# Optimization experiments

Hardware: AMD Instinct MI355X
Metric: run time of the kernel (lower is better)

The kernel has to match this reference:

```python
import jax, jax.numpy as jnp
import numpy as np

T, D_IN, D_OUT, E, K = 4096, 1024, 1024, 8, 2
H = max(D_IN, D_OUT) * 4  # 4096, per nbHidden = max(nbIn, nbOut) * 4


def setup_inputs() -> dict:
    key = jax.random.key(0)
    ks = jax.random.split(key, 12)
    s = 0.02
    return {
        "x": jax.random.normal(ks[0], (T, D_IN), dtype=jnp.float32),
        "noise": jax.random.normal(ks[1], (T, E), dtype=jnp.float32),
        "gate_w": jax.random.normal(ks[2], (D_IN, E), dtype=jnp.float32) * s,
        "gate_b": jnp.zeros((E,), dtype=jnp.float32),
        "noise_w": jax.random.normal(ks[3], (D_IN, E), dtype=jnp.float32) * s,
        "noise_b": jnp.zeros((E,), dtype=jnp.float32),
        "w1": jax.random.normal(ks[4], (E, D_IN, H), dtype=jnp.float32) * s,
        "b1": jnp.zeros((E, H), dtype=jnp.float32),
        "w2": jax.random.normal(ks[5], (E, H, D_OUT), dtype=jnp.float32) * s,
        "b2": jnp.zeros((E, D_OUT), dtype=jnp.float32),
    }


def reference(x, noise, gate_w, gate_b, noise_w, noise_b, w1, b1, w2, b2):
    # Noisy gating: gate(x) + randn * softplus(noise(x))
    logits = (x @ gate_w + gate_b) + noise * jax.nn.softplus(x @ noise_w + noise_b)  # [T, E]
    topk_vals, topk_idx = jax.lax.top_k(logits, K)          # [T, K]
    gate_prob = jax.nn.softmax(topk_vals, axis=1)           # softmax over selected K logits
    rows = jnp.arange(x.shape[0])[:, None]
    weights = jnp.zeros((x.shape[0], E), dtype=x.dtype).at[rows, topk_idx].set(gate_prob)  # [T, E]

    # Dense path (memMode=False): run every expert MLP on all tokens, masked combine.
    h = jax.nn.relu(jnp.einsum("ti,eih->teh", x, w1) + b1[None])   # [T, E, H]
    expert_out = jnp.einsum("teh,eho->teo", h, w2) + b2[None]       # [T, E, O]
    x_out = jnp.einsum("te,teo->to", weights, expert_out)           # [T, O]
    return x_out, weights
```

## Files before the change

kernel.cpp:

```cpp
#include <hip/hip_runtime.h>

#define T_TOK 4096
#define DIN   1024
#define DOUT  1024
#define NEXP  8
#define HDIM  4096
#define RCAP  9216
#define MT128 80

typedef float f32x4 __attribute__((ext_vector_type(4)));
typedef short bf16x8 __attribute__((ext_vector_type(8)));
typedef unsigned short u16x4 __attribute__((ext_vector_type(4)));
typedef unsigned short u16x8 __attribute__((ext_vector_type(8)));

__device__ __forceinline__ float bf2f(unsigned short u) {
    union { unsigned int i; float f; } v; v.i = ((unsigned int)u) << 16; return v.f;
}
__device__ __forceinline__ unsigned short f2bf(float f) {
    union { unsigned int i; float f; } v; v.f = f;
    unsigned int r = v.i + 0x7FFFu + ((v.i >> 16) & 1u);
    return (unsigned short)(r >> 16);
}

__global__ __launch_bounds__(64) void gating_kernel(
    const float* __restrict__ x, const float* __restrict__ noise,
    const float* __restrict__ gw, const float* __restrict__ gb,
    const float* __restrict__ nw, const float* __restrict__ nb,
    float* __restrict__ wout,
    int* __restrict__ tok_e, float* __restrict__ tok_p)
{
    int t = blockIdx.x;
    int lane = threadIdx.x;
    const float* xr = x + (size_t)t * DIN;
    double ag[NEXP], an[NEXP];
#pragma unroll
    for (int e = 0; e < NEXP; ++e) { ag[e] = 0.0; an[e] = 0.0; }
    for (int d = lane; d < DIN; d += 64) {
        double xv = (double)xr[d];
        const f32x4* g4 = (const f32x4*)(gw + (size_t)d * NEXP);
        const f32x4* n4 = (const f32x4*)(nw + (size_t)d * NEXP);
        f32x4 ga = g4[0], gbv = g4[1], na = n4[0], nbv = n4[1];
#pragma unroll
        for (int j = 0; j < 4; ++j) {
            ag[j]     += xv * (double)ga[j];
            ag[4 + j] += xv * (double)gbv[j];
            an[j]     += xv * (double)na[j];
            an[4 + j] += xv * (double)nbv[j];
        }
    }
#pragma unroll
    for (int e = 0; e < NEXP; ++e) {
        double g = ag[e], n = an[e];
#pragma unroll
        for (int m = 32; m > 0; m >>= 1) { g += __shfl_xor(g, m); n += __shfl_xor(n, m); }
        ag[e] = g; an[e] = n;
    }
    double lg[NEXP];
#pragma unroll
    for (int e = 0; e < NEXP; ++e) {
        double z = an[e] + (double)nb[e];
        double sp = fmax(z, 0.0) + log1p(exp(-fabs(z)));
        lg[e] = ag[e] + (double)gb[e] + (double)noise[(size_t)t * NEXP + e] * sp;
    }
    int i0 = 0; double v0 = lg[0];
#pragma unroll
    for (int e = 1; e < NEXP; ++e) if (lg[e] > v0) { v0 = lg[e]; i0 = e; }
    int i1 = -1; double v1 = -1.0e300;
#pragma unroll
    for (int e = 0; e < NEXP; ++e) if (e != i0 && lg[e] > v1) { v1 = lg[e]; i1 = e; }
    double d1 = exp(v1 - v0);
    float p0 = (float)(1.0 / (1.0 + d1));
    float p1 = (float)(d1 / (1.0 + d1));
    if (lane < NEXP) {
        float wv = (lane == i0) ? p0 : ((lane == i1) ? p1 : 0.0f);
        wout[(size_t)t * NEXP + lane] = wv;
    }
    if (lane == 0) {
        tok_e[2 * t] = i0;     tok_e[2 * t + 1] = i1;
        tok_p[2 * t] = p0;     tok_p[2 * t + 1] = p1;
    }
}

__global__ __launch_bounds__(256) void scan_kernel(
    const int* __restrict__ tok_e, int* __restrict__ tok_slot, int* __restrict__ cnt)
{
    __shared__ int wsum[4];
    int e = blockIdx.x;
    int tid = threadIdx.x;
    int wv = tid >> 6;
    int lane = tid & 63;
    int base = 0;
    for (int c = 0; c < 2 * T_TOK; c += 256) {
        int i = c + tid;
        int m = (tok_e[i] == e) ? 1 : 0;
        unsigned long long bal = __ballot(m);
        int before = __popcll(bal & ((1ull << lane) - 1ull));
        if (lane == 0) wsum[wv] = __popcll(bal);
        __syncthreads();
        int woff = 0;
#pragma unroll
        for (int w = 0; w < 4; ++w) if (w < wv) woff += wsum[w];
        if (m) tok_slot[i] = base + woff + before;
        int tot = wsum[0] + wsum[1] + wsum[2] + wsum[3];
        __syncthreads();
        base += tot;
    }
    if (tid == 0) cnt[e] = base;
}

__global__ void prefix_kernel(const int* __restrict__ cnt, int* __restrict__ poff,
                              int* __restrict__ t2e, int* __restrict__ trow)
{
    if (threadIdx.x != 0 || blockIdx.x != 0) return;
    int base = 0, a = 0;
    for (int e = 0; e < NEXP; ++e) {
        poff[e] = base;
        int c = cnt[e];
        int nt = (c + 127) >> 7;
        for (int i = 0; i < nt; ++i) { t2e[a] = e; trow[a] = base + (i << 7); ++a; }
        base += nt << 7;
    }
    for (; a < MT128; ++a) { t2e[a] = -1; trow[a] = 0; }
}

__global__ __launch_bounds__(256) void gather_kernel(
    const float* __restrict__ x, const int* __restrict__ tok_e,
    const int* __restrict__ tok_slot, const int* __restrict__ poff,
    unsigned short* __restrict__ Xg)
{
    int b = blockIdx.x;
    int t = b >> 1, k = b & 1;
    int e = tok_e[2 * t + k];
    int row = poff[e] + tok_slot[2 * t + k];
    int c = threadIdx.x << 2;
    f32x4 v = *(const f32x4*)(x + (size_t)t * DIN + c);
    u16x4 o;
#pragma unroll
    for (int j = 0; j < 4; ++j) o[j] = f2bf(v[j]);
    *(u16x4*)(Xg + (size_t)row * DIN + c) = o;
}

__global__ __launch_bounds__(256) void convw2x_kernel(
    const float* __restrict__ w1, unsigned short* __restrict__ W1t,
    const float* __restrict__ w2, unsigned short* __restrict__ W2t)
{
    __shared__ float tile[64][65];
    int e = blockIdx.x;
    int idx = blockIdx.y;
    const float* W; unsigned short* Wt; int K, N, k0, n0;
    if (idx < 1024) {
        W = w1; Wt = W1t; K = DIN; N = HDIM;
        k0 = (idx >> 6) << 6; n0 = (idx & 63) << 6;
    } else {
        int i2 = idx - 1024;
        W = w2; Wt = W2t; K = HDIM; N = DOUT;
        k0 = (i2 >> 4) << 6; n0 = (i2 & 15) << 6;
    }
    int tid = threadIdx.x;
    const float* src = W + ((size_t)e * K + k0) * N + n0;
    int r = tid >> 4, c4 = (tid & 15) << 2;
#pragma unroll
    for (int i = 0; i < 4; ++i) {
        f32x4 v = *(const f32x4*)(src + (size_t)(r + (i << 4)) * N + c4);
        *(f32x4*)(&tile[r + (i << 4)][c4]) = v;
    }
    __syncthreads();
    unsigned short* dst = Wt + ((size_t)e * N + n0) * K + k0;
#pragma unroll
    for (int i = 0; i < 2; ++i) {
        int u = (i << 8) + tid;
        int n = u >> 3, kk = (u & 7) << 3;
        u16x8 o;
#pragma unroll
        for (int q = 0; q < 8; ++q) o[q] = f2bf(tile[kk + q][n]);
        *(u16x8*)(dst + (size_t)n * K + kk) = o;
    }
}

__global__ __launch_bounds__(512, 4) void gemm1_wide_kernel(
    const unsigned short* __restrict__ A,
    const unsigned short* __restrict__ Bt,
    unsigned short* __restrict__ C,
    const float* __restrict__ bias,
    const int* __restrict__ t2e, const int* __restrict__ trow)
{
    const int lda = DIN, ldb = DIN, N = HDIM;
    int cpx = gridDim.x >> 3;
    int wg = ((blockIdx.x & 7) * cpx) + (blockIdx.x >> 3);
    int tileid = wg >> 4;
    int nb = wg & 15;
    int e = t2e[tileid];
    if (e < 0) return;
    int row0 = trow[tileid];
    int n0 = nb << 8;

    __shared__ __align__(16) unsigned short As[128 * 64];
    __shared__ __align__(16) unsigned short Bs[256 * 64];

    int tid = threadIdx.x;
    int lane = tid & 63;
    int wv = tid >> 6;
    int wr = (wv >> 2) << 6;
    int wc = (wv & 3) << 6;

    const unsigned short* Ab = A + (size_t)row0 * lda;
    const unsigned short* Bb = Bt + ((size_t)e * N + n0) * ldb;

    f32x4 acc[4][4] = {};
    int hr = lane & 15;
    int q4 = lane >> 4;

    for (int kt = 0; kt < 16; ++kt) {
        __syncthreads();
        int kb = kt << 6;
#pragma unroll
        for (int i = 0; i < 2; ++i) {
            int u = (i << 9) + tid;
            int r = u >> 3, sp = u & 7;
            int col = ((sp ^ (r & 7)) << 3);
            __builtin_amdgcn_global_load_lds(
                (const __attribute__((address_space(1))) void*)(Ab + (size_t)r * lda + kb + col),
                (__attribute__((address_space(3))) void*)(&As[u << 3]), 16, 0, 0);
        }
#pragma unroll
        for (int i = 0; i < 4; ++i) {
            int u = (i << 9) + tid;
            int r = u >> 3, sp = u & 7;
            int col = ((sp ^ (r & 7)) << 3);
            __builtin_amdgcn_global_load_lds(
                (const __attribute__((address_space(1))) void*)(Bb + (size_t)r * ldb + kb + col),
                (__attribute__((address_space(3))) void*)(&Bs[u << 3]), 16, 0, 0);
        }
        __syncthreads();
#pragma unroll
        for (int kq = 0; kq < 2; ++kq) {
            int slog = (kq << 2) | q4;
            bf16x8 af[4], bfv[4];
#pragma unroll
            for (int m = 0; m < 4; ++m) {
                int r = wr + (m << 4) + hr;
                af[m] = *(const bf16x8*)(&As[(r << 6) + ((slog ^ (r & 7)) << 3)]);
            }
#pragma unroll
            for (int n = 0; n < 4; ++n) {
                int r = wc + (n << 4) + hr;
                bfv[n] = *(const bf16x8*)(&Bs[(r << 6) + ((slog ^ (r & 7)) << 3)]);
            }
#pragma unroll
            for (int m = 0; m < 4; ++m)
#pragma unroll
                for (int n = 0; n < 4; ++n)
                    acc[m][n] = __builtin_amdgcn_mfma_f32_16x16x32_bf16(af[m], bfv[n], acc[m][n], 0, 0, 0);
        }
    }

    int rq = q4 << 2;
    int cl = hr;
#pragma unroll
    for (int n = 0; n < 4; ++n) {
        int col = wc + (n << 4) + cl;
        float bv = bias[(size_t)e * N + n0 + col];
#pragma unroll
        for (int m = 0; m < 4; ++m) {
#pragma unroll
            for (int r = 0; r < 4; ++r) {
                int row = wr + (m << 4) + rq + r;
                float v = acc[m][n][r] + bv;
                v = fmaxf(v, 0.0f);
                C[(size_t)(row0 + row) * N + n0 + col] = f2bf(v);
            }
        }
    }
}

__global__ __launch_bounds__(256, 4) void gemm64_kernel(
    const unsigned short* __restrict__ A, int lda,
    const unsigned short* __restrict__ Bt, int ldb, int N, int KLEN,
    unsigned short* __restrict__ C,
    const float* __restrict__ bias,
    const int* __restrict__ t2e, const int* __restrict__ trow,
    int nbshift, int relu)
{
    int nwg = gridDim.x;
    int cpx = nwg >> 3;
    int wg = ((blockIdx.x & 7) * cpx) + (blockIdx.x >> 3);
    int tileid = wg >> nbshift;
    int nb = wg & ((1 << nbshift) - 1);

    int e = t2e[tileid];
    if (e < 0) return;
    int row0 = trow[tileid];
    int n0 = nb << 7;

    __shared__ __align__(16) unsigned short As[128 * 64];
    __shared__ __align__(16) unsigned short Bs[128 * 64];

    int tid = threadIdx.x;
    int lane = tid & 63;
    int wv = tid >> 6;
    int wr = (wv >> 1) << 6;
    int wc = (wv & 1) << 6;

    const unsigned short* Ab = A + (size_t)row0 * lda;
    const unsigned short* Bb = Bt + ((size_t)e * N + n0) * ldb;

    f32x4 acc[4][4] = {};

    int sr_lo = tid >> 3;
    int sp = tid & 7;
    int hr = lane & 15;
    int q4 = lane >> 4;

    int nkt = KLEN >> 6;
    for (int kt = 0; kt < nkt; ++kt) {
        __syncthreads();
        int kb = kt << 6;
#pragma unroll
        for (int i = 0; i < 4; ++i) {
            int r = (i << 5) + sr_lo;
            int col = ((sp ^ (r & 7)) << 3);
            int u = (i << 8) + tid;
            __builtin_amdgcn_global_load_lds(
                (const __attribute__((address_space(1))) void*)(Ab + (size_t)r * lda + kb + col),
                (__attribute__((address_space(3))) void*)(&As[u << 3]), 16, 0, 0);
            __builtin_amdgcn_global_load_lds(
                (const __attribute__((address_space(1))) void*)(Bb + (size_t)r * ldb + kb + col),
                (__attribute__((address_space(3))) void*)(&Bs[u << 3]), 16, 0, 0);
        }
        __syncthreads();
#pragma unroll
        for (int kq = 0; kq < 2; ++kq) {
            int slog = (kq << 2) | q4;
            bf16x8 af[4], bfv[4];
#pragma unroll
            for (int m = 0; m < 4; ++m) {
                int r = wr + (m << 4) + hr;
                af[m] = *(const bf16x8*)(&As[(r << 6) + ((slog ^ (r & 7)) << 3)]);
            }
#pragma unroll
            for (int n = 0; n < 4; ++n) {
                int r = wc + (n << 4) + hr;
                bfv[n] = *(const bf16x8*)(&Bs[(r << 6) + ((slog ^ (r & 7)) << 3)]);
            }
#pragma unroll
            for (int m = 0; m < 4; ++m)
#pragma unroll
                for (int n = 0; n < 4; ++n)
                    acc[m][n] = __builtin_amdgcn_mfma_f32_16x16x32_bf16(af[m], bfv[n], acc[m][n], 0, 0, 0);
        }
    }

    int rq = q4 << 2;
    int cl = hr;
#pragma unroll
    for (int n = 0; n < 4; ++n) {
        int col = wc + (n << 4) + cl;
        float bv = bias[(size_t)e * N + n0 + col];
#pragma unroll
        for (int m = 0; m < 4; ++m) {
#pragma unroll
            for (int r = 0; r < 4; ++r) {
                int row = wr + (m << 4) + rq + r;
                float v = acc[m][n][r] + bv;
                if (relu) v = fmaxf(v, 0.0f);
                C[(size_t)(row0 + row) * N + n0 + col] = f2bf(v);
            }
        }
    }
}

__global__ __launch_bounds__(256) void combine_kernel(
    const unsigned short* __restrict__ O, const int* __restrict__ tok_e,
    const int* __restrict__ tok_slot, const float* __restrict__ tok_p,
    const int* __restrict__ poff, float* __restrict__ xout)
{
    int t = blockIdx.x;
    int e0 = tok_e[2 * t], e1 = tok_e[2 * t + 1];
    int r0 = poff[e0] + tok_slot[2 * t];
    int r1 = poff[e1] + tok_slot[2 * t + 1];
    float p0 = tok_p[2 * t], p1 = tok_p[2 * t + 1];
    int c = threadIdx.x << 2;
    u16x4 a = *(const u16x4*)(O + (size_t)r0 * DOUT + c);
    u16x4 b = *(const u16x4*)(O + (size_t)r1 * DOUT + c);
    f32x4 r;
#pragma unroll
    for (int j = 0; j < 4; ++j) r[j] = p0 * bf2f(a[j]) + p1 * bf2f(b[j]);
    *(f32x4*)(xout + (size_t)t * DOUT + c) = r;
}

extern "C" void kernel_launch(void* const* d_in, const int* in_sizes, int n_in,
                              void* d_out, int out_size, void* d_ws, size_t ws_size,
                              hipStream_t stream)
{
    const float* x     = (const float*)d_in[0];
    const float* noise = (const float*)d_in[1];
    const float* gw    = (const float*)d_in[2];
    const float* gb    = (const float*)d_in[3];
    const float* nw    = (const float*)d_in[4];
    const float* nb    = (const float*)d_in[5];
    const float* w1    = (const float*)d_in[6];
    const float* b1    = (const float*)d_in[7];
    const float* w2    = (const float*)d_in[8];
    const float* b2    = (const float*)d_in[9];
    float* xout = (float*)d_out;
    float* wout = xout + (size_t)T_TOK * DOUT;

    char* ws = (char*)d_ws;
    int*   cnt      = (int*)(ws + 0);
    int*   poff     = (int*)(ws + 256);
    int*   t2e      = (int*)(ws + 512);
    int*   trow     = (int*)(ws + 1024);
    int*   tok_e    = (int*)(ws + 2048);
    int*   tok_slot = (int*)(ws + 34816);
    float* tok_p    = (float*)(ws + 67584);
    size_t oXg = 104448;
    unsigned short* Xg  = (unsigned short*)(ws + oXg);
    unsigned short* O   = Xg;
    size_t oH  = oXg + (size_t)RCAP * DIN * 2;
    unsigned short* H   = (unsigned short*)(ws + oH);
    size_t oW1 = oH + (size_t)RCAP * HDIM * 2;
    unsigned short* W1t = (unsigned short*)(ws + oW1);
    size_t oW2 = oW1 + (size_t)NEXP * HDIM * DIN * 2;
    unsigned short* W2t = (unsigned short*)(ws + oW2);

    gating_kernel<<<T_TOK, 64, 0, stream>>>(x, noise, gw, gb, nw, nb,
                                            wout, tok_e, tok_p);
    scan_kernel<<<NEXP, 256, 0, stream>>>(tok_e, tok_slot, cnt);
    prefix_kernel<<<1, 1, 0, stream>>>(cnt, poff, t2e, trow);
    gather_kernel<<<2 * T_TOK, 256, 0, stream>>>(x, tok_e, tok_slot, poff, Xg);
    convw2x_kernel<<<dim3(NEXP, 2048), 256, 0, stream>>>(w1, W1t, w2, W2t);
    gemm1_wide_kernel<<<MT128 * 16, 512, 0, stream>>>(
        Xg, W1t, H, b1, t2e, trow);
    gemm64_kernel<<<MT128 * 8, 256, 0, stream>>>(
        H, HDIM, W2t, HDIM, DOUT, HDIM, O, b2, t2e, trow, 3, 0);
    combine_kernel<<<T_TOK, 256, 0, stream>>>(O, tok_e, tok_slot, tok_p, poff, xout);
}
```

Measured before the change: 335.1 us.

## Split-K the second expert GEMM and fold gating into weight-conversion kernel

The second grouped GEMM is split into two K halves, doubling its workgroup count. Each half writes bf16 partials into scratch buffers that reuse the W1t region, and the combine kernel adds them. Separately, the gating computation is folded into the weight transpose/convert kernel as extra grid rows, removing one launch and letting gating overlap with conversion. The cost is extra partial-output traffic and a second bf16 rounding of each partial sum.

```diff
diff --git a/kernel.cpp b/kernel.cpp
--- a/kernel.cpp
+++ b/kernel.cpp
@@ -22,15 +22,13 @@
     return (unsigned short)(r >> 16);
 }
 
-__global__ __launch_bounds__(64) void gating_kernel(
+__device__ __forceinline__ void gating_body(
+    int t, int lane,
     const float* __restrict__ x, const float* __restrict__ noise,
     const float* __restrict__ gw, const float* __restrict__ gb,
     const float* __restrict__ nw, const float* __restrict__ nb,
-    float* __restrict__ wout,
-    int* __restrict__ tok_e, float* __restrict__ tok_p)
-{
-    int t = blockIdx.x;
-    int lane = threadIdx.x;
+    float* __restrict__ wout, int* __restrict__ tok_e, float* __restrict__ tok_p)
+{
     const float* xr = x + (size_t)t * DIN;
     double ag[NEXP], an[NEXP];
 #pragma unroll
@@ -78,6 +76,52 @@
     if (lane == 0) {
         tok_e[2 * t] = i0;     tok_e[2 * t + 1] = i1;
         tok_p[2 * t] = p0;     tok_p[2 * t + 1] = p1;
+    }
+}
+
+__global__ __launch_bounds__(256) void prep_kernel(
+    const float* __restrict__ w1, unsigned short* __restrict__ W1t,
+    const float* __restrict__ w2, unsigned short* __restrict__ W2t,
+    const float* __restrict__ x, const float* __restrict__ noise,
+    const float* __restrict__ gw, const float* __restrict__ gb,
+    const float* __restrict__ nw, const float* __restrict__ nb,
+    float* __restrict__ wout, int* __restrict__ tok_e, float* __restrict__ tok_p)
+{
+    __shared__ float tile[64][65];
+    int yy = blockIdx.y;
+    int tid = threadIdx.x;
+    if (yy >= 2048) {
+        int t = (((yy - 2048) << 3) + blockIdx.x) * 4 + (tid >> 6);
+        gating_body(t, tid & 63, x, noise, gw, gb, nw, nb, wout, tok_e, tok_p);
+        return;
+    }
+    int e = blockIdx.x;
+    const float* W; unsigned short* Wt; int K, N, k0, n0;
+    if (yy < 1024) {
+        W = w1; Wt = W1t; K = DIN; N = HDIM;
+        k0 = (yy >> 6) << 6; n0 = (yy & 63) << 6;
+    } else {
+        int i2 = yy - 1024;
+        W = w2; Wt = W2t; K = HDIM; N = DOUT;
+        k0 = (i2 >> 4) << 6; n0 = (i2 & 15) << 6;
+    }
+    const float* src = W + ((size_t)e * K + k0) * N + n0;
+    int r = tid >> 4, c4 = (tid & 15) << 2;
+#pragma unroll
+    for (int i = 0; i < 4; ++i) {
+        f32x4 v = *(const f32x4*)(src + (size_t)(r + (i << 4)) * N + c4);
+        *(f32x4*)(&tile[r + (i << 4)][c4]) = v;
+    }
+    __syncthreads();
+    unsigned short* dst = Wt + ((size_t)e * N + n0) * K + k0;
+#pragma unroll
+    for (int i = 0; i < 2; ++i) {
+        int u = (i << 8) + tid;
+        int n = u >> 3, kk = (u & 7) << 3;
+        u16x8 o;
+#pragma unroll
+        for (int q = 0; q < 8; ++q) o[q] = f2bf(tile[kk + q][n]);
+        *(u16x8*)(dst + (size_t)n * K + kk) = o;
     }
 }
 
@@ -140,43 +184,6 @@
     *(u16x4*)(Xg + (size_t)row * DIN + c) = o;
 }
 
-__global__ __launch_bounds__(256) void convw2x_kernel(
-    const float* __restrict__ w1, unsigned short* __restrict__ W1t,
-    const float* __restrict__ w2, unsigned short* __restrict__ W2t)
-{
-    __shared__ float tile[64][65];
-    int e = blockIdx.x;
-    int idx = blockIdx.y;
-    const float* W; unsigned short* Wt; int K, N, k0, n0;
-    if (idx < 1024) {
-        W = w1; Wt = W1t; K = DIN; N = HDIM;
-        k0 = (idx >> 6) << 6; n0 = (idx & 63) << 6;
-    } else {
-        int i2 = idx - 1024;
-        W = w2; Wt = W2t; K = HDIM; N = DOUT;
-        k0 = (i2 >> 4) << 6; n0 = (i2 & 15) << 6;
-    }
-    int tid = threadIdx.x;
-    const float* src = W + ((size_t)e * K + k0) * N + n0;
-    int r = tid >> 4, c4 = (tid & 15) << 2;
-#pragma unroll
-    for (int i = 0; i < 4; ++i) {
-        f32x4 v = *(const f32x4*)(src + (size_t)(r + (i << 4)) * N + c4);
-        *(f32x4*)(&tile[r + (i << 4)][c4]) = v;
-    }
-    __syncthreads();
-    unsigned short* dst = Wt + ((size_t)e * N + n0) * K + k0;
-#pragma unroll
-    for (int i = 0; i < 2; ++i) {
-        int u = (i << 8) + tid;
-        int n = u >> 3, kk = (u & 7) << 3;
-        u16x8 o;
-#pragma unroll
-        for (int q = 0; q < 8; ++q) o[q] = f2bf(tile[kk + q][n]);
-        *(u16x8*)(dst + (size_t)n * K + kk) = o;
-    }
-}
-
 __global__ __launch_bounds__(512, 4) void gemm1_wide_kernel(
     const unsigned short* __restrict__ A,
     const unsigned short* __restrict__ Bt,
@@ -273,24 +280,27 @@
     }
 }
 
-__global__ __launch_bounds__(256, 4) void gemm64_kernel(
-    const unsigned short* __restrict__ A, int lda,
-    const unsigned short* __restrict__ Bt, int ldb, int N, int KLEN,
-    unsigned short* __restrict__ C,
+__global__ __launch_bounds__(256, 4) void gemm2_sk_kernel(
+    const unsigned short* __restrict__ A,
+    const unsigned short* __restrict__ Bt,
+    unsigned short* __restrict__ C0, unsigned short* __restrict__ C1,
     const float* __restrict__ bias,
-    const int* __restrict__ t2e, const int* __restrict__ trow,
-    int nbshift, int relu)
-{
-    int nwg = gridDim.x;
-    int cpx = nwg >> 3;
+    const int* __restrict__ t2e, const int* __restrict__ trow)
+{
+    const int lda = HDIM, ldb = HDIM, N = DOUT, KLEN = HDIM / 2;
+    int cpx = gridDim.x >> 3;
     int wg = ((blockIdx.x & 7) * cpx) + (blockIdx.x >> 3);
-    int tileid = wg >> nbshift;
-    int nb = wg & ((1 << nbshift) - 1);
+    int tileid = wg >> 4;
+    int low = wg & 15;
+    int nb = low >> 1;
+    int ks = low & 1;
 
     int e = t2e[tileid];
     if (e < 0) return;
     int row0 = trow[tileid];
     int n0 = nb << 7;
+    int koff = ks * KLEN;
+    unsigned short* C = ks ? C1 : C0;
 
     __shared__ __align__(16) unsigned short As[128 * 64];
     __shared__ __align__(16) unsigned short Bs[128 * 64];
@@ -301,8 +311,8 @@
     int wr = (wv >> 1) << 6;
     int wc = (wv & 1) << 6;
 
-    const unsigned short* Ab = A + (size_t)row0 * lda;
-    const unsigned short* Bb = Bt + ((size_t)e * N + n0) * ldb;
+    const unsigned short* Ab = A + (size_t)row0 * lda + koff;
+    const unsigned short* Bb = Bt + ((size_t)e * N + n0) * ldb + koff;
 
     f32x4 acc[4][4] = {};
 
@@ -311,8 +321,7 @@
     int hr = lane & 15;
     int q4 = lane >> 4;
 
-    int nkt = KLEN >> 6;
-    for (int kt = 0; kt < nkt; ++kt) {
+    for (int kt = 0; kt < KLEN / 64; ++kt) {
         __syncthreads();
         int kb = kt << 6;
 #pragma unroll
@@ -355,24 +364,23 @@
 #pragma unroll
     for (int n = 0; n < 4; ++n) {
         int col = wc + (n << 4) + cl;
-        float bv = bias[(size_t)e * N + n0 + col];
+        float bv = (ks == 0) ? bias[(size_t)e * N + n0 + col] : 0.0f;
 #pragma unroll
         for (int m = 0; m < 4; ++m) {
 #pragma unroll
             for (int r = 0; r < 4; ++r) {
                 int row = wr + (m << 4) + rq + r;
-                float v = acc[m][n][r] + bv;
-                if (relu) v = fmaxf(v, 0.0f);
-                C[(size_t)(row0 + row) * N + n0 + col] = f2bf(v);
+                C[(size_t)(row0 + row) * N + n0 + col] = f2bf(acc[m][n][r] + bv);
             }
         }
     }
 }
 
 __global__ __launch_bounds__(256) void combine_kernel(
-    const unsigned short* __restrict__ O, const int* __restrict__ tok_e,
-    const int* __restrict__ tok_slot, const float* __restrict__ tok_p,
-    const int* __restrict__ poff, float* __restrict__ xout)
+    const unsigned short* __restrict__ Oa, const unsigned short* __restrict__ Ob,
+    const int* __restrict__ tok_e, const int* __restrict__ tok_slot,
+    const float* __restrict__ tok_p, const int* __restrict__ poff,
+    float* __restrict__ xout)
 {
     int t = blockIdx.x;
     int e0 = tok_e[2 * t], e1 = tok_e[2 * t + 1];
@@ -380,11 +388,14 @@
     int r1 = poff[e1] + tok_slot[2 * t + 1];
     float p0 = tok_p[2 * t], p1 = tok_p[2 * t + 1];
     int c = threadIdx.x << 2;
-    u16x4 a = *(const u16x4*)(O + (size_t)r0 * DOUT + c);
-    u16x4 b = *(const u16x4*)(O + (size_t)r1 * DOUT + c);
+    u16x4 a0 = *(const u16x4*)(Oa + (size_t)r0 * DOUT + c);
+    u16x4 a1 = *(const u16x4*)(Ob + (size_t)r0 * DOUT + c);
+    u16x4 b0 = *(const u16x4*)(Oa + (size_t)r1 * DOUT + c);
+    u16x4 b1 = *(const u16x4*)(Ob + (size_t)r1 * DOUT + c);
     f32x4 r;
 #pragma unroll
-    for (int j = 0; j < 4; ++j) r[j] = p0 * bf2f(a[j]) + p1 * bf2f(b[j]);
+    for (int j = 0; j < 4; ++j)
+        r[j] = p0 * (bf2f(a0[j]) + bf2f(a1[j])) + p1 * (bf2f(b0[j]) + bf2f(b1[j]));
     *(f32x4*)(xout + (size_t)t * DOUT + c) = r;
 }
 
@@ -415,23 +426,23 @@
     float* tok_p    = (float*)(ws + 67584);
     size_t oXg = 104448;
     unsigned short* Xg  = (unsigned short*)(ws + oXg);
-    unsigned short* O   = Xg;
     size_t oH  = oXg + (size_t)RCAP * DIN * 2;
     unsigned short* H   = (unsigned short*)(ws + oH);
     size_t oW1 = oH + (size_t)RCAP * HDIM * 2;
     unsigned short* W1t = (unsigned short*)(ws + oW1);
     size_t oW2 = oW1 + (size_t)NEXP * HDIM * DIN * 2;
     unsigned short* W2t = (unsigned short*)(ws + oW2);
-
-    gating_kernel<<<T_TOK, 64, 0, stream>>>(x, noise, gw, gb, nw, nb,
-                                            wout, tok_e, tok_p);
+    unsigned short* Oa = W1t;
+    unsigned short* Ob = W1t + (size_t)RCAP * DOUT;
+
+    prep_kernel<<<dim3(NEXP, 2176), 256, 0, stream>>>(
+        w1, W1t, w2, W2t, x, noise, gw, gb, nw, nb, wout, tok_e, tok_p);
     scan_kernel<<<NEXP, 256, 0, stream>>>(tok_e, tok_slot, cnt);
     prefix_kernel<<<1, 1, 0, stream>>>(cnt, poff, t2e, trow);
     gather_kernel<<<2 * T_TOK, 256, 0, stream>>>(x, tok_e, tok_slot, poff, Xg);
-    convw2x_kernel<<<dim3(NEXP, 2048), 256, 0, stream>>>(w1, W1t, w2, W2t);
     gemm1_wide_kernel<<<MT128 * 16, 512, 0, stream>>>(
         Xg, W1t, H, b1, t2e, trow);
-    gemm64_kernel<<<MT128 * 8, 256, 0, stream>>>(
-        H, HDIM, W2t, HDIM, DOUT, HDIM, O, b2, t2e, trow, 3, 0);
-    combine_kernel<<<T_TOK, 256, 0, stream>>>(O, tok_e, tok_slot, tok_p, poff, xout);
-}
+    gemm2_sk_kernel<<<MT128 * 16, 256, 0, stream>>>(
+        H, W2t, Oa, Ob, b2, t2e, trow);
+    combine_kernel<<<T_TOK, 256, 0, stream>>>(Oa, Ob, tok_e, tok_slot, tok_p, poff, xout);
+}
```

Result: no change. 338.9 us (+1.1%).
